# Kernel optimization log

Hardware: AMD Instinct MI355X
Metric: run time of the kernel (lower is better)

The kernel has to match this reference:

```python
import jax, jax.numpy as jnp
import numpy as np

B, C, T, H, W, TS = 4, 512, 2048, 8, 16, 1000
D = C // H  # head_dim = 64
SCALE = D ** -0.5


def _conv1x1(w, b, z):
    # torch Conv1d(dim, dim, 1): (B,C,T) -> (B,C,T)
    return jnp.einsum('oc,bct->bot', w, z) + b[None, :, None]


def _linear(w, b, z):
    # torch Linear: z @ w.T + b, w is (out,in)
    return z @ w.T + b


def _rope(x, cos, sin):
    # x: (B,H,T,D); cos/sin: (T, D//2) broadcast over (B,H)
    x1, x2 = x[..., ::2], x[..., 1::2]
    r = jnp.stack([x1 * cos - x2 * sin, x1 * sin + x2 * cos], axis=-1)
    return r.reshape(x.shape)


def _local(x, cond, qw, qb, kw, kb, vw, vb, ow, ob):
    q = _conv1x1(qw, qb, x)
    k = _conv1x1(kw, kb, cond)
    v = _conv1x1(vw, vb, cond)
    pl = W // 2
    pr = W - pl - 1
    kp = jnp.pad(k, ((0, 0), (0, 0), (pl, pr)))
    vp = jnp.pad(v, ((0, 0), (0, 0), (pl, pr)))
    idx = jnp.arange(T)[:, None] + jnp.arange(W)[None, :]  # (T,W)
    ku = kp[:, :, idx].reshape(B, H, D, T, W)
    vu = vp[:, :, idx].reshape(B, H, D, T, W)
    qh = q.reshape(B, H, D, T)
    dots = jnp.einsum('bhdt,bhdtw->bhtw', qh, ku) * SCALE
    attn = jax.nn.softmax(dots, axis=-1)
    out = jnp.einsum('bhtw,bhdtw->bhdt', attn, vu)
    # faithful to torch: permute(0,1,3,2).contiguous().view(B,C,T)
    out = out.transpose(0, 1, 3, 2).reshape(B, C, T)
    return _conv1x1(ow, ob, out)


def _global(xg, cg, qw, qb, kw, kb, vw, vb, ow, ob):
    # xg, cg: (B,T,C)
    q = _linear(qw, qb, xg).reshape(B, T, H, D).transpose(0, 2, 1, 3)
    k = _linear(kw, kb, cg).reshape(B, T, H, D).transpose(0, 2, 1, 3)
    v = _linear(vw, vb, cg).reshape(B, T, H, D).transpose(0, 2, 1, 3)
    inv_freq = 1.0 / (10000.0 ** (jnp.arange(0, D, 2, dtype=jnp.float32) / D))
    pos = jnp.arange(T, dtype=jnp.float32)
    sinus = pos[:, None] * inv_freq[None, :]  # (T, D//2)
    cos, sin = jnp.cos(sinus), jnp.sin(sinus)
    q = _rope(q, cos, sin)
    k = _rope(k, cos, sin)
    dots = jnp.einsum('bhqd,bhkd->bhqk', q, k) * SCALE
    attn = jax.nn.softmax(dots, axis=-1)
    out = jnp.einsum('bhqk,bhkd->bhqd', attn, v)
    out = out.transpose(0, 2, 1, 3).reshape(B, T, C)
    return _linear(ow, ob, out)


def setup_inputs() -> dict:
    key = jax.random.key(0)
    ks = jax.random.split(key, 20)
    pm = lambda k: jax.random.normal(k, (C, C), dtype=jnp.float32) * 0.02
    pb = lambda k: jax.random.normal(k, (C,), dtype=jnp.float32) * 0.02
    return {
        'x': jax.random.normal(ks[0], (B, C, T), dtype=jnp.float32),
        'cond': jax.random.normal(ks[1], (B, C, T), dtype=jnp.float32),
        't': jax.random.randint(ks[2], (B,), 0, TS),
        'lq_w': pm(ks[3]), 'lq_b': pb(ks[4]),
        'lk_w': pm(ks[5]), 'lk_b': pb(ks[6]),
        'lv_w': pm(ks[7]), 'lv_b': pb(ks[8]),
        'lo_w': pm(ks[9]), 'lo_b': pb(ks[10]),
        'gq_w': pm(ks[11]), 'gq_b': pb(ks[12]),
        'gk_w': pm(ks[13]), 'gk_b': pb(ks[14]),
        'gv_w': pm(ks[15]), 'gv_b': pb(ks[16]),
        'go_w': pm(ks[17]), 'go_b': pb(ks[18]),
    }


def reference(x, cond, t, lq_w, lq_b, lk_w, lk_b, lv_w, lv_b, lo_w, lo_b,
              gq_w, gq_b, gk_w, gk_b, gv_w, gv_b, go_w, go_b):
    ctx_local = _local(x, cond, lq_w, lq_b, lk_w, lk_b, lv_w, lv_b, lo_w, lo_b)
    ctx_global = _global(x.transpose(0, 2, 1), cond.transpose(0, 2, 1),
                         gq_w, gq_b, gk_w, gk_b, gv_w, gv_b, go_w, go_b)
    ctx_global = ctx_global.transpose(0, 2, 1)  # (B,C,T)
    t_norm = t.astype(jnp.float32) / jnp.float32(TS - 1)
    a_g = (1.0 - t_norm)[:, None, None]
    a_l = t_norm[:, None, None]
    return jnp.sqrt(a_g) * ctx_global + jnp.sqrt(a_l) * ctx_local
```

## Files before the change

kernel.cpp:

```cpp
#include <hip/hip_runtime.h>
#include <math.h>

#define BB 4
#define CC 512
#define TT 2048
#define HH 8
#define DD 64

static constexpr float SCALE = 0.125f;
static constexpr float QK_SCALE_LOG2 = 0.125f * 1.4426950408889634f;

typedef __attribute__((ext_vector_type(8)))  short  short8;
typedef __attribute__((ext_vector_type(4)))  float  f32x4;
typedef __attribute__((ext_vector_type(16))) float  f32x16;
typedef __attribute__((ext_vector_type(2)))  unsigned int u32x2;

static __device__ __forceinline__ ushort f2bf(float f) {
    uint u = __float_as_uint(f);
    uint r = (u + 0x7fffu + ((u >> 16) & 1u)) >> 16;
    return (ushort)r;
}
static __device__ __forceinline__ float bf2f(ushort u) {
    return __uint_as_float((uint)u << 16);
}

typedef unsigned int u32;
typedef u32 __attribute__((address_space(1))) gu32;
typedef u32 __attribute__((address_space(3))) lu32;
static __device__ __forceinline__ void gload_lds16(const void* g, void* l) {
    __builtin_amdgcn_global_load_lds((const gu32*)g, (lu32*)l, 16, 0, 0);
}

__global__ __launch_bounds__(256)
void prep_kernel(const float* __restrict__ x, const float* __restrict__ cond,
                 const float* w0, const float* w1, const float* w2, const float* w3,
                 const float* w4, const float* w5, const float* w6, const float* w7,
                 ushort* __restrict__ wbf, ushort* __restrict__ wc,
                 ushort* __restrict__ xtb, ushort* __restrict__ ctb,
                 float* __restrict__ ctab, float* __restrict__ stab)
{
    __shared__ ushort L[64][66];
    int bid = blockIdx.x;
    const int tid = threadIdx.x;

    if (bid < 256) {
        int idx = bid * 256 + tid;
        int i = idx >> 11;
        int t = idx & 2047;
        float ex   = (2.0f * (float)i) / 64.0f;
        float invf = powf(10000.0f, -ex);
        float ang  = (float)t * invf;
        ctab[idx] = cosf(ang);
        stab[idx] = sinf(ang);
        return;
    }
    bid -= 256;
    if (bid < 2048) {
        const float* srcs[8] = {w0, w1, w2, w3, w4, w5, w6, w7};
        int wi = bid >> 8;
        int idx = ((bid & 255) * 256 + tid) * 4;
        float4 v = *(const float4*)&srcs[wi][idx];
        uint lo = (uint)f2bf(v.x) | ((uint)f2bf(v.y) << 16);
        uint hi = (uint)f2bf(v.z) | ((uint)f2bf(v.w) << 16);
        uint2 pk = make_uint2(lo, hi);
        if (wi < 6) {
            *(uint2*)&wbf[(size_t)wi * 262144 + idx] = pk;
        } else {
            int row = idx >> 9, col = idx & 511;
            *(uint2*)&wc[(size_t)row * 1024 + (wi - 6) * 512 + col] = pk;
        }
        return;
    }
    bid -= 2048;
    const int z = bid >> 8;
    const int r = bid & 255;
    const float* in = (z < 4) ? x : cond;
    ushort* outp    = (z < 4) ? xtb : ctb;
    const int b = z & 3;
    const int t0 = (r & 31) * 64, c0 = (r >> 5) * 64;
    const float* inb = in + (size_t)b * CC * TT;
    ushort* outb = outp + (size_t)b * TT * CC;
    const int lc = tid >> 6;
    const int lt = tid & 63;
    #pragma unroll
    for (int i = 0; i < 16; i++) {
        int c = i * 4 + lc;
        L[c][lt] = f2bf(inb[(size_t)(c0 + c) * TT + t0 + lt]);
    }
    __syncthreads();
    #pragma unroll
    for (int i = 0; i < 16; i++) {
        int t = i * 4 + lc;
        outb[(size_t)(t0 + t) * CC + c0 + lt] = L[lt][t];
    }
}

__global__ __launch_bounds__(256)
void transpose_bf16_kernel(const ushort* __restrict__ in, ushort* __restrict__ AG)
{
    __shared__ ushort L[64][66];
    const int t0 = blockIdx.x * 64, c0 = blockIdx.y * 64, b = blockIdx.z;
    const ushort* inb = in + (size_t)b * CC * TT;
    ushort* outb = AG + (size_t)b * TT * 1024;
    const int lc = threadIdx.x >> 6;
    const int lt = threadIdx.x & 63;
    #pragma unroll
    for (int i = 0; i < 16; i++) {
        int c = i * 4 + lc;
        L[c][lt] = inb[(size_t)(c0 + c) * TT + t0 + lt];
    }
    __syncthreads();
    #pragma unroll
    for (int i = 0; i < 16; i++) {
        int t = i * 4 + lc;
        outb[(size_t)(t0 + t) * 1024 + c0 + lt] = L[lt][t];
    }
}

#define GEMM_BODY(Wp, XTp, KD, NB)                                                  \
    __shared__ __align__(16) ushort As[2][128][32];                                 \
    __shared__ __align__(16) ushort Bs[2][NB][32];                                  \
    const int tid  = threadIdx.x;                                                   \
    const int wid  = tid >> 6;                                                      \
    const int lane = tid & 63;                                                      \
    const int x  = lane & 15;                                                       \
    const int gq = lane >> 4;                                                       \
    const int wm = wid >> 1, wn = wid & 1;                                          \
    const int m0 = blockIdx.y * 128;                                                \
    const int n0 = blockIdx.x * NB;                                                 \
    const int srow = lane >> 2;                                                     \
    const int sblk = lane & 3;                                                      \
    f32x4 acc[4][NB / 32];                                                          \
    _Pragma("unroll")                                                               \
    for (int i = 0; i < 4; i++)                                                     \
        _Pragma("unroll")                                                           \
        for (int j = 0; j < NB / 32; j++) acc[i][j] = (f32x4){0.f, 0.f, 0.f, 0.f};  \
    auto stage = [&](int bf, int k0) {                                              \
        _Pragma("unroll")                                                           \
        for (int c = 0; c < 2; c++) {                                               \
            int row = c * 64 + wid * 16 + srow;                                     \
            int dbk = sblk ^ ((row >> 1) & 3);                                      \
            gload_lds16(&Wp[(size_t)(m0 + row) * KD + k0 + dbk * 8],                \
                        &As[bf][c * 64 + wid * 16][0]);                             \
            if (c * 64 < NB)                                                        \
                gload_lds16(&XTp[(size_t)(n0 + row) * KD + k0 + dbk * 8],           \
                            &Bs[bf][c * 64 + wid * 16][0]);                         \
        }                                                                           \
    };                                                                              \
    stage(0, 0);                                                                    \
    __syncthreads();                                                                \
    for (int ks = 0; ks < (KD) / 32; ks++) {                                        \
        int cur = ks & 1;                                                           \
        if (ks < (KD) / 32 - 1) stage(cur ^ 1, (ks + 1) * 32);                      \
        short8 aF[4], bF[NB / 32];                                                  \
        _Pragma("unroll")                                                           \
        for (int mi = 0; mi < 4; mi++) {                                            \
            int row = wm * 64 + mi * 16 + x;                                        \
            aF[mi] = *(const short8*)&As[cur][row][(gq ^ ((row >> 1) & 3)) * 8];    \
        }                                                                           \
        _Pragma("unroll")                                                           \
        for (int nj = 0; nj < NB / 32; nj++) {                                      \
            int row = wn * (NB / 2) + nj * 16 + x;                                  \
            bF[nj] = *(const short8*)&Bs[cur][row][(gq ^ ((row >> 1) & 3)) * 8];    \
        }                                                                           \
        _Pragma("unroll")                                                           \
        for (int mi = 0; mi < 4; mi++)                                              \
            _Pragma("unroll")                                                       \
            for (int nj = 0; nj < NB / 32; nj++)                                    \
                acc[mi][nj] = __builtin_amdgcn_mfma_f32_16x16x32_bf16(aF[mi], bF[nj], acc[mi][nj], 0, 0, 0); \
        __syncthreads();                                                            \
    }

__global__ __launch_bounds__(256)
void gemm6_kernel(const ushort* __restrict__ wbase,
                  const float* __restrict__ b0, const float* __restrict__ b1, const float* __restrict__ b2,
                  const float* __restrict__ b3, const float* __restrict__ b4, const float* __restrict__ b5,
                  const ushort* __restrict__ xtb, const ushort* __restrict__ ctb,
                  ushort* __restrict__ y0, ushort* __restrict__ y1, ushort* __restrict__ y2,
                  ushort* __restrict__ y3, ushort* __restrict__ y4, ushort* __restrict__ y5,
                  const float* __restrict__ ctab, const float* __restrict__ stab)
{
    const int z = blockIdx.z;
    const ushort* Wp  = wbase + (size_t)z * 262144;
    const float* bias = (z == 0) ? b0 : (z == 1) ? b1 : (z == 2) ? b2 : (z == 3) ? b3 : (z == 4) ? b4 : b5;
    const ushort* XTp = (z == 0 || z == 3) ? xtb : ctb;
    ushort* Y = (z == 0) ? y0 : (z == 1) ? y1 : (z == 2) ? y2 : (z == 3) ? y3 : (z == 4) ? y4 : y5;
    const bool do_rope = (z == 3 || z == 4);
    const float qscale = (z == 3) ? QK_SCALE_LOG2 : 1.0f;

    GEMM_BODY(Wp, XTp, 512, 128)

    const int bidx = (n0 + wn * 64) >> 11;
    #pragma unroll
    for (int mi = 0; mi < 4; mi++) {
        const int mb = m0 + wm * 64 + mi * 16 + 4 * gq;
        float bv[4];
        #pragma unroll
        for (int r = 0; r < 4; r++) bv[r] = bias[mb + r];
        #pragma unroll
        for (int nj = 0; nj < 4; nj++) {
            const int n  = n0 + wn * 64 + nj * 16 + x;
            const int tt = n & 2047;
            f32x4 v = acc[mi][nj];
            v[0] += bv[0]; v[1] += bv[1]; v[2] += bv[2]; v[3] += bv[3];
            if (do_rope) {
                const int i0 = (mb & 63) >> 1;
                float c0 = ctab[(size_t)i0 * 2048 + tt],       s0 = stab[(size_t)i0 * 2048 + tt];
                float c1 = ctab[(size_t)(i0 + 1) * 2048 + tt], s1 = stab[(size_t)(i0 + 1) * 2048 + tt];
                float e0 = (v[0] * c0 - v[1] * s0) * qscale;
                float e1 = (v[0] * s0 + v[1] * c0) * qscale;
                float e2 = (v[2] * c1 - v[3] * s1) * qscale;
                float e3 = (v[2] * s1 + v[3] * c1) * qscale;
                v[0] = e0; v[1] = e1; v[2] = e2; v[3] = e3;
            }
            if (z <= 3) {
                uint lo = (uint)f2bf(v[0]) | ((uint)f2bf(v[1]) << 16);
                uint hi = (uint)f2bf(v[2]) | ((uint)f2bf(v[3]) << 16);
                *(uint2*)&Y[(size_t)n * 512 + mb] = make_uint2(lo, hi);
            } else if (z == 4) {
                const int hh = (mb >> 6) & 7;
                const int d  = mb & 63;
                const int kap = d >> 4, hb = (d >> 3) & 1, j0 = d & 7;
                const int kt = tt >> 6, tk = tt & 63, sb = tk >> 5, qh = tk & 31;
                size_t off = ((size_t)(bidx * 8 + hh)) * 131072
                           + (size_t)(((((kt * 2 + sb) * 4 + kap) * 2 + hb) * 32 + qh) * 8 + j0);
                uint lo = (uint)f2bf(v[0]) | ((uint)f2bf(v[1]) << 16);
                uint hi = (uint)f2bf(v[2]) | ((uint)f2bf(v[3]) << 16);
                *(uint2*)&Y[off] = make_uint2(lo, hi);
            } else {
                const int hh = (mb >> 6) & 7;
                const int qh0 = mb & 31, db = (mb & 63) >> 5;
                const int kt = tt >> 6, kk = tt & 63;
                const int kc = kk >> 4, hb = (kk >> 3) & 1, j = kk & 7;
                size_t base = ((size_t)(bidx * 8 + hh)) * 131072
                            + (size_t)(((((kt * 2 + db) * 4 + kc) * 2 + hb) * 32 + qh0) * 8 + j);
                #pragma unroll
                for (int r = 0; r < 4; r++)
                    Y[base + (size_t)r * 8] = f2bf(v[r]);
            }
        }
    }
}

__global__ __launch_bounds__(256)
void gemm_comb_kernel(const ushort* __restrict__ Wp,
                      const float* __restrict__ bl, const float* __restrict__ bg,
                      const ushort* __restrict__ XTp, float* __restrict__ Y,
                      const int* __restrict__ tarr)
{
    GEMM_BODY(Wp, XTp, 1024, 64)

    const int bidx = (n0 + wn * 32) >> 11;
    float tn = (float)tarr[bidx] / 999.0f;
    float sl = sqrtf(tn), sg = sqrtf(1.0f - tn);

    #pragma unroll
    for (int mi = 0; mi < 4; mi++) {
        const int mb = m0 + wm * 64 + mi * 16 + 4 * gq;
        float bv[4];
        #pragma unroll
        for (int r = 0; r < 4; r++) bv[r] = sl * bl[mb + r] + sg * bg[mb + r];
        #pragma unroll
        for (int nj = 0; nj < 2; nj++) {
            const int tt = (n0 + wn * 32 + nj * 16 + x) & 2047;
            f32x4 v = acc[mi][nj];
            #pragma unroll
            for (int r = 0; r < 4; r++)
                Y[((size_t)bidx * 512 + mb + r) * 2048 + tt] = v[r] + bv[r];
        }
    }
}

__global__ __launch_bounds__(256)
void local_attn_kernel(const ushort* __restrict__ qt, const ushort* __restrict__ kt,
                       const ushort* __restrict__ vt, ushort* __restrict__ outb,
                       const int* __restrict__ tarr)
{
    int gidx = blockIdx.x * 256 + threadIdx.x;
    int t  = gidx & (TT - 1);
    int bh = gidx >> 11;
    int h  = bh & (HH - 1);
    int b  = bh >> 3;
    const size_t rb = (size_t)b * TT;
    const int co = h * DD;
    const float wl = sqrtf((float)tarr[b] / 999.0f);

    float qf[64];
    {
        const ushort* qp = qt + (rb + t) * 512 + co;
        #pragma unroll
        for (int i = 0; i < 8; i++) {
            short8 v = *(const short8*)&qp[i * 8];
            #pragma unroll
            for (int j = 0; j < 8; j++) qf[i * 8 + j] = bf2f((ushort)v[j]);
        }
    }

    int koff[16]; float msk[16];
    #pragma unroll
    for (int w = 0; w < 16; w++) {
        int kidx = t + w - 8;
        msk[w]  = (kidx >= 0 && kidx < TT) ? 1.0f : 0.0f;
        koff[w] = min(max(kidx, 0), TT - 1);
    }

    float dots[16];
    #pragma unroll
    for (int w = 0; w < 16; w++) {
        const ushort* kp = kt + (rb + koff[w]) * 512 + co;
        float d0 = 0.f, d1 = 0.f;
        #pragma unroll
        for (int i = 0; i < 8; i++) {
            short8 v = *(const short8*)&kp[i * 8];
            #pragma unroll
            for (int j = 0; j < 8; j += 2) {
                d0 = fmaf(qf[i * 8 + j],     bf2f((ushort)v[j]),     d0);
                d1 = fmaf(qf[i * 8 + j + 1], bf2f((ushort)v[j + 1]), d1);
            }
        }
        dots[w] = d0 + d1;
    }

    float m = -1e30f;
    #pragma unroll
    for (int w = 0; w < 16; w++) { dots[w] = dots[w] * SCALE * msk[w]; m = fmaxf(m, dots[w]); }
    float p[16], s = 0.f;
    #pragma unroll
    for (int w = 0; w < 16; w++) { p[w] = __expf(dots[w] - m); s += p[w]; }
    float inv = wl / s;
    #pragma unroll
    for (int w = 0; w < 16; w++) p[w] *= msk[w] * inv;

    float oa[64];
    #pragma unroll
    for (int d = 0; d < 64; d++) oa[d] = 0.f;
    #pragma unroll
    for (int w = 0; w < 16; w++) {
        const ushort* vp = vt + (rb + koff[w]) * 512 + co;
        #pragma unroll
        for (int i = 0; i < 8; i++) {
            short8 v = *(const short8*)&vp[i * 8];
            #pragma unroll
            for (int j = 0; j < 8; j++)
                oa[i * 8 + j] = fmaf(p[w], bf2f((ushort)v[j]), oa[i * 8 + j]);
        }
    }

    ushort* op = outb + ((size_t)b * CC + co + (t >> 5)) * TT + (size_t)(t & 31) * DD;
    #pragma unroll
    for (int i = 0; i < 16; i++) {
        uint lo = (uint)f2bf(oa[i * 4 + 0]) | ((uint)f2bf(oa[i * 4 + 1]) << 16);
        uint hi = (uint)f2bf(oa[i * 4 + 2]) | ((uint)f2bf(oa[i * 4 + 3]) << 16);
        *(uint2*)&op[i * 4] = make_uint2(lo, hi);
    }
}

__global__ __launch_bounds__(64)
void flash_global_kernel(const ushort* __restrict__ qtd, const ushort* __restrict__ KT,
                         const ushort* __restrict__ VT, ushort* __restrict__ AG,
                         const int* __restrict__ tarr)
{
    const int lane = threadIdx.x;
    const int qh = lane & 31;

    const int bid = blockIdx.x;
    const int sw  = (bid & 7) * 256 + (bid >> 3);
    const int qt  = sw & 63;
    const int p   = sw >> 6;
    const int hh  = p & 7, b = p >> 3;

    const size_t kvbase = (size_t)p * 131072;
    const size_t btd    = (size_t)b * TT;
    const int q_glob = qt * 32 + qh;
    const float sg_mix = sqrtf(1.0f - (float)tarr[b] / 999.0f);

    const ushort* Kb = KT + kvbase;
    const ushort* Vb = VT + kvbase;

    short8 aQ[4];
    {
        const int h = lane >> 5;
        const ushort* qrow = qtd + (btd + q_glob) * 512 + hh * 64;
        #pragma unroll
        for (int kap = 0; kap < 4; kap++)
            aQ[kap] = *(const short8*)&qrow[kap * 16 + h * 8];
    }

    f32x16 oacc[2];
    #pragma unroll
    for (int d = 0; d < 2; d++)
        #pragma unroll
        for (int r = 0; r < 16; r++) oacc[d][r] = 0.f;
    float l_run = 0.0f;

    short8 kf[8], vf[8];
    auto loadK = [&](int kt) {
        #pragma unroll
        for (int i = 0; i < 8; i++)
            kf[i] = *(const short8*)&Kb[(size_t)(kt * 8 + i) * 512 + lane * 8];
    };
    auto loadV = [&](int kt) {
        #pragma unroll
        for (int i = 0; i < 8; i++)
            vf[i] = *(const short8*)&Vb[(size_t)(kt * 8 + i) * 512 + lane * 8];
    };
    loadK(0);
    loadV(0);

    for (int kt = 0; kt < 32; kt++) {
        f32x16 ST[2];
        #pragma unroll
        for (int sb = 0; sb < 2; sb++)
            #pragma unroll
            for (int r = 0; r < 16; r++) ST[sb][r] = 0.f;
        __builtin_amdgcn_s_setprio(1);
        #pragma unroll
        for (int sb = 0; sb < 2; sb++)
            #pragma unroll
            for (int kap = 0; kap < 4; kap++)
                ST[sb] = __builtin_amdgcn_mfma_f32_32x32x16_bf16(kf[sb * 4 + kap], aQ[kap], ST[sb], 0, 0, 0);
        __builtin_amdgcn_s_setprio(0);

        if (kt < 31) loadK(kt + 1);

        float s0 = 0.f, s1 = 0.f, s2 = 0.f, s3 = 0.f;
        #pragma unroll
        for (int sb = 0; sb < 2; sb++)
            #pragma unroll
            for (int r = 0; r < 16; r += 4) {
                ST[sb][r + 0] = __builtin_amdgcn_exp2f(ST[sb][r + 0]);
                ST[sb][r + 1] = __builtin_amdgcn_exp2f(ST[sb][r + 1]);
                ST[sb][r + 2] = __builtin_amdgcn_exp2f(ST[sb][r + 2]);
                ST[sb][r + 3] = __builtin_amdgcn_exp2f(ST[sb][r + 3]);
                s0 += ST[sb][r + 0]; s1 += ST[sb][r + 1];
                s2 += ST[sb][r + 2]; s3 += ST[sb][r + 3];
            }
        l_run += (s0 + s1) + (s2 + s3);

        short8 bP[4];
        #pragma unroll
        for (int sb = 0; sb < 2; sb++)
            #pragma unroll
            for (int kcp = 0; kcp < 2; kcp++) {
                const int rb2 = kcp * 8;
                uint ca, cb, cc, cd;
                asm("v_cvt_pk_bf16_f32 %0, %1, %2" : "=v"(ca) : "v"(ST[sb][rb2 + 0]), "v"(ST[sb][rb2 + 1]));
                asm("v_cvt_pk_bf16_f32 %0, %1, %2" : "=v"(cb) : "v"(ST[sb][rb2 + 2]), "v"(ST[sb][rb2 + 3]));
                asm("v_cvt_pk_bf16_f32 %0, %1, %2" : "=v"(cc) : "v"(ST[sb][rb2 + 4]), "v"(ST[sb][rb2 + 5]));
                asm("v_cvt_pk_bf16_f32 %0, %1, %2" : "=v"(cd) : "v"(ST[sb][rb2 + 6]), "v"(ST[sb][rb2 + 7]));
                u32x2 r1 = __builtin_amdgcn_permlane32_swap(ca, cc, false, false);
                u32x2 r2 = __builtin_amdgcn_permlane32_swap(cb, cd, false, false);
                uint4 bu = make_uint4(r1[0], r2[0], r1[1], r2[1]);
                bP[sb * 2 + kcp] = __builtin_bit_cast(short8, bu);
            }

        __builtin_amdgcn_s_setprio(1);
        #pragma unroll
        for (int db = 0; db < 2; db++)
            #pragma unroll
            for (int kc = 0; kc < 4; kc++)
                oacc[db] = __builtin_amdgcn_mfma_f32_32x32x16_bf16(vf[db * 4 + kc], bP[kc], oacc[db], 0, 0, 0);
        __builtin_amdgcn_s_setprio(0);

        if (kt < 31) loadV(kt + 1);
    }

    const int h = lane >> 5;
    float ltot = l_run + __shfl_xor(l_run, 32);
    float inv = sg_mix / ltot;
    ushort* agrow = AG + (btd + q_glob) * 1024 + 512 + hh * 64;
    #pragma unroll
    for (int db = 0; db < 2; db++)
        #pragma unroll
        for (int rq = 0; rq < 4; rq++) {
            const int d0 = db * 32 + rq * 8 + h * 4;
            uint lo = (uint)f2bf(oacc[db][rq * 4 + 0] * inv) | ((uint)f2bf(oacc[db][rq * 4 + 1] * inv) << 16);
            uint hi = (uint)f2bf(oacc[db][rq * 4 + 2] * inv) | ((uint)f2bf(oacc[db][rq * 4 + 3] * inv) << 16);
            *(uint2*)&agrow[d0] = make_uint2(lo, hi);
        }
}

extern "C" void kernel_launch(void* const* d_in, const int* in_sizes, int n_in,
                              void* d_out, int out_size, void* d_ws, size_t ws_size,
                              hipStream_t stream)
{
    const float* x    = (const float*)d_in[0];
    const float* cond = (const float*)d_in[1];
    const int*   tarr = (const int*)d_in[2];
    const float* lq_w = (const float*)d_in[3];
    const float* lq_b = (const float*)d_in[4];
    const float* lk_w = (const float*)d_in[5];
    const float* lk_b = (const float*)d_in[6];
    const float* lv_w = (const float*)d_in[7];
    const float* lv_b = (const float*)d_in[8];
    const float* lo_w = (const float*)d_in[9];
    const float* lo_b = (const float*)d_in[10];
    const float* gq_w = (const float*)d_in[11];
    const float* gq_b = (const float*)d_in[12];
    const float* gk_w = (const float*)d_in[13];
    const float* gk_b = (const float*)d_in[14];
    const float* gv_w = (const float*)d_in[15];
    const float* gv_b = (const float*)d_in[16];
    const float* go_w = (const float*)d_in[17];
    const float* go_b = (const float*)d_in[18];
    float* out = (float*)d_out;

    const size_t N = (size_t)BB * CC * TT;
    char* w = (char*)d_ws;
    ushort* xtb = (ushort*)w; w += N * 2;
    ushort* ctb = (ushort*)w; w += N * 2;
    ushort* lq  = (ushort*)w; w += N * 2;
    ushort* lk  = (ushort*)w; w += N * 2;
    ushort* lv  = (ushort*)w; w += N * 2;
    ushort* gqb = (ushort*)w; w += N * 2;
    ushort* ktb = (ushort*)w; w += N * 2;
    ushort* vtb = (ushort*)w; w += N * 2;
    ushort* scr = (ushort*)w; w += N * 2;
    ushort* AG  = (ushort*)w; w += (size_t)BB * TT * 1024 * 2;
    ushort* wbf = (ushort*)w; w += (size_t)6 * 512 * 512 * 2;
    ushort* wc  = (ushort*)w; w += (size_t)512 * 1024 * 2;
    float* ctab = (float*)w;  w += (size_t)32 * 2048 * 4;
    float* stab = (float*)w;

    dim3 blk(256);

    prep_kernel<<<dim3(4352), blk, 0, stream>>>(x, cond,
                                                lq_w, lk_w, lv_w, gq_w, gk_w, gv_w, lo_w, go_w,
                                                wbf, wc, xtb, ctb, ctab, stab);

    gemm6_kernel<<<dim3(64, 4, 6), blk, 0, stream>>>(wbf, lq_b, lk_b, lv_b, gq_b, gk_b, gv_b,
                                                     xtb, ctb, lq, lk, lv, gqb, ktb, vtb, ctab, stab);

    local_attn_kernel<<<dim3(BB * HH * TT / 256), blk, 0, stream>>>(lq, lk, lv, scr, tarr);
    transpose_bf16_kernel<<<dim3(32, 8, BB), blk, 0, stream>>>(scr, AG);

    flash_global_kernel<<<dim3(2048), dim3(64), 0, stream>>>(gqb, ktb, vtb, AG, tarr);

    gemm_comb_kernel<<<dim3(128, 4), blk, 0, stream>>>(wc, lo_b, go_b, AG, out, tarr);
}
```

Measured before the change: 177.7 us.

## Share K/V tiles across four waves via double-buffered LDS in global flash attention

The flash global attention kernel changes from one wave per 32-query block, each loading K/V straight from global memory into registers, to 256-thread blocks of four waves covering 128 queries. The waves share K/V tiles staged in LDS through direct global-to-LDS loads with double buffering. This cuts global/L2 traffic for K and V by a factor of four and frees registers. In exchange it adds a block-wide barrier per tile and LDS read latency before each MFMA, and it launches a quarter as many blocks.

```diff
diff --git a/kernel.cpp b/kernel.cpp
--- a/kernel.cpp
+++ b/kernel.cpp
@@ -355,23 +355,29 @@
     }
 }
 
-__global__ __launch_bounds__(64)
+__global__ __launch_bounds__(256)
 void flash_global_kernel(const ushort* __restrict__ qtd, const ushort* __restrict__ KT,
                          const ushort* __restrict__ VT, ushort* __restrict__ AG,
                          const int* __restrict__ tarr)
 {
-    const int lane = threadIdx.x;
-    const int qh = lane & 31;
+    __shared__ __align__(16) ushort Ks[2][4096];
+    __shared__ __align__(16) ushort Vs[2][4096];
+
+    const int tid  = threadIdx.x;
+    const int w    = tid >> 6;
+    const int lane = tid & 63;
+    const int qh   = lane & 31;
+    const int h    = lane >> 5;
 
     const int bid = blockIdx.x;
-    const int sw  = (bid & 7) * 256 + (bid >> 3);
-    const int qt  = sw & 63;
-    const int p   = sw >> 6;
+    const int sw  = (bid & 7) * 64 + (bid >> 3);
+    const int qt  = sw & 15;
+    const int p   = sw >> 4;
     const int hh  = p & 7, b = p >> 3;
 
     const size_t kvbase = (size_t)p * 131072;
     const size_t btd    = (size_t)b * TT;
-    const int q_glob = qt * 32 + qh;
+    const int q_glob = qt * 128 + w * 32 + qh;
     const float sg_mix = sqrtf(1.0f - (float)tarr[b] / 999.0f);
 
     const ushort* Kb = KT + kvbase;
@@ -379,7 +385,6 @@
 
     short8 aQ[4];
     {
-        const int h = lane >> 5;
         const ushort* qrow = qtd + (btd + q_glob) * 512 + hh * 64;
         #pragma unroll
         for (int kap = 0; kap < 4; kap++)
@@ -393,21 +398,26 @@
         for (int r = 0; r < 16; r++) oacc[d][r] = 0.f;
     float l_run = 0.0f;
 
-    short8 kf[8], vf[8];
-    auto loadK = [&](int kt) {
-        #pragma unroll
-        for (int i = 0; i < 8; i++)
-            kf[i] = *(const short8*)&Kb[(size_t)(kt * 8 + i) * 512 + lane * 8];
+    const ushort* kA = Kb + (size_t)(2 * w) * 512 + lane * 8;
+    const ushort* vA = Vb + (size_t)(2 * w) * 512 + lane * 8;
+
+    auto issue = [&](int buf, int kt) {
+        const size_t off = (size_t)kt * 4096;
+        gload_lds16(kA + off,       &Ks[buf][(2 * w) * 512]);
+        gload_lds16(kA + off + 512, &Ks[buf][(2 * w + 1) * 512]);
+        gload_lds16(vA + off,       &Vs[buf][(2 * w) * 512]);
+        gload_lds16(vA + off + 512, &Vs[buf][(2 * w + 1) * 512]);
     };
-    auto loadV = [&](int kt) {
-        #pragma unroll
-        for (int i = 0; i < 8; i++)
-            vf[i] = *(const short8*)&Vb[(size_t)(kt * 8 + i) * 512 + lane * 8];
-    };
-    loadK(0);
-    loadV(0);
-
+    issue(0, 0);
+
+    int cur = 0;
     for (int kt = 0; kt < 32; kt++) {
+        __syncthreads();
+        if (kt < 31) issue(cur ^ 1, kt + 1);
+
+        const ushort* KsC = &Ks[cur][0];
+        const ushort* VsC = &Vs[cur][0];
+
         f32x16 ST[2];
         #pragma unroll
         for (int sb = 0; sb < 2; sb++)
@@ -417,11 +427,11 @@
         #pragma unroll
         for (int sb = 0; sb < 2; sb++)
             #pragma unroll
-            for (int kap = 0; kap < 4; kap++)
-                ST[sb] = __builtin_amdgcn_mfma_f32_32x32x16_bf16(kf[sb * 4 + kap], aQ[kap], ST[sb], 0, 0, 0);
+            for (int kap = 0; kap < 4; kap++) {
+                short8 aK = *(const short8*)&KsC[(sb * 4 + kap) * 512 + lane * 8];
+                ST[sb] = __builtin_amdgcn_mfma_f32_32x32x16_bf16(aK, aQ[kap], ST[sb], 0, 0, 0);
+            }
         __builtin_amdgcn_s_setprio(0);
-
-        if (kt < 31) loadK(kt + 1);
 
         float s0 = 0.f, s1 = 0.f, s2 = 0.f, s3 = 0.f;
         #pragma unroll
@@ -458,14 +468,14 @@
         #pragma unroll
         for (int db = 0; db < 2; db++)
             #pragma unroll
-            for (int kc = 0; kc < 4; kc++)
-                oacc[db] = __builtin_amdgcn_mfma_f32_32x32x16_bf16(vf[db * 4 + kc], bP[kc], oacc[db], 0, 0, 0);
+            for (int kc = 0; kc < 4; kc++) {
+                short8 aV = *(const short8*)&VsC[(db * 4 + kc) * 512 + lane * 8];
+                oacc[db] = __builtin_amdgcn_mfma_f32_32x32x16_bf16(aV, bP[kc], oacc[db], 0, 0, 0);
+            }
         __builtin_amdgcn_s_setprio(0);
-
-        if (kt < 31) loadV(kt + 1);
-    }
-
-    const int h = lane >> 5;
+        cur ^= 1;
+    }
+
     float ltot = l_run + __shfl_xor(l_run, 32);
     float inv = sg_mix / ltot;
     ushort* agrow = AG + (btd + q_glob) * 1024 + 512 + hh * 64;
@@ -534,7 +544,7 @@
     local_attn_kernel<<<dim3(BB * HH * TT / 256), blk, 0, stream>>>(lq, lk, lv, scr, tarr);
     transpose_bf16_kernel<<<dim3(32, 8, BB), blk, 0, stream>>>(scr, AG);
 
-    flash_global_kernel<<<dim3(2048), dim3(64), 0, stream>>>(gqb, ktb, vtb, AG, tarr);
+    flash_global_kernel<<<dim3(512), blk, 0, stream>>>(gqb, ktb, vtb, AG, tarr);
 
     gemm_comb_kernel<<<dim3(128, 4), blk, 0, stream>>>(wc, lo_b, go_b, AG, out, tarr);
 }
```

Result: no change. 177.5 us (-0.1%).
